# Performance work log

Hardware: AMD Instinct MI355X
Metric: run time of the kernel (lower is better)

Reference implementation:

```python
import jax, jax.numpy as jnp
import numpy as np

NUM_CLASSES = 3
WINDOW = 5.0        # window_size for local connectivity
NUM_ITERS = 5       # mean-field iterations
THETA_BETA = 1.0    # smoothness kernel weight
TEMP = 1.0          # softmax temperature
H, W = 96, 96
B = 1


def setup_inputs() -> dict:
    key = jax.random.key(0)
    unary = jax.random.normal(key, (B, NUM_CLASSES, H, W), dtype=jnp.float32)
    # nn.Parameter(torch.eye(num_classes))
    compatibility = jnp.eye(NUM_CLASSES, dtype=jnp.float32)
    return {"unary": unary, "compatibility": compatibility}


def _pairwise_kernel(h, w):
    """Dense smoothness * local-connectivity kernel [N, N], N = h*w."""
    yy, xx = jnp.meshgrid(jnp.arange(h, dtype=jnp.float32),
                          jnp.arange(w, dtype=jnp.float32), indexing='ij')
    coords = jnp.stack([yy.ravel(), xx.ravel()], axis=-1)          # [N, 2]
    diff = coords[:, None, :] - coords[None, :, :]                 # [N, N, 2]
    dist = jnp.sqrt(jnp.sum(diff * diff, axis=-1))                 # cdist, [N, N]
    n = h * w
    conn = (dist <= WINDOW).astype(jnp.float32)
    conn = conn.at[jnp.arange(n), jnp.arange(n)].set(0.0)          # fill_diagonal_(0)
    smooth = jnp.exp(-THETA_BETA * dist)
    return smooth * conn                                           # [N, N]


def reference(unary, compatibility):
    b, c, h, w = unary.shape
    n = h * w
    unary_flat = unary.reshape(b, c, n)                            # [B, C, N]
    q = jax.nn.softmax(unary_flat / TEMP, axis=1)
    pairwise = _pairwise_kernel(h, w)                              # [N, N] (features=None path)
    for _ in range(NUM_ITERS):
        # messages[b,c,n] = sum_m pairwise[n,m] * q[b,c,m]  (bmm + transpose)
        messages = jnp.einsum('nm,bcm->bcn', pairwise, q)
        comp_msg = jnp.einsum('cd,bdn->bcn', compatibility, messages)
        q = jax.nn.softmax((unary_flat + comp_msg) / TEMP, axis=1)
    return q.reshape(b, c, h, w)
```

## Files before the change

kernel.cpp:

```cpp
#include <hip/hip_runtime.h>


constexpr int HH = 96, WW = 96, NN = HH * WW;
constexpr int TILE = 16, HALO = 5, EXT = TILE + 2 * HALO;

template <bool FIRST, bool LAST>
__global__ __launch_bounds__(TILE * TILE) void crf_iter(
    const float* __restrict__ unary,
    const float* __restrict__ comp,
    const float4* __restrict__ zin,
    float4* __restrict__ zout,
    float* __restrict__ qout)
{
    __shared__ float4 qs[EXT][EXT];
    __shared__ float wtab[121];

    const int tx = threadIdx.x, ty = threadIdx.y;
    const int tid = ty * TILE + tx;

    if (tid < 121) {
        int dy = tid / 11 - 5, dx = tid % 11 - 5;
        int d2 = dy * dy + dx * dx;
        wtab[tid] = (d2 > 0 && d2 <= 25) ? expf(-sqrtf((float)d2)) : 0.0f;
    }

    const int bx0 = blockIdx.x * TILE, by0 = blockIdx.y * TILE;

    for (int i = tid; i < EXT * EXT; i += TILE * TILE) {
        int hy = i / EXT, hx = i - hy * EXT;
        int gy = by0 + hy - HALO, gx = bx0 + hx - HALO;
        float4 q = make_float4(0.f, 0.f, 0.f, 0.f);
        if (gy >= 0 && gy < HH && gx >= 0 && gx < WW) {
            int n = gy * WW + gx;
            float z0, z1, z2;
            if (FIRST) {
                z0 = unary[n];
                z1 = unary[NN + n];
                z2 = unary[2 * NN + n];
            } else {
                float4 z = zin[n];
                z0 = z.x; z1 = z.y; z2 = z.z;
            }
            float mx = fmaxf(z0, fmaxf(z1, z2));
            float e0 = expf(z0 - mx), e1 = expf(z1 - mx), e2 = expf(z2 - mx);
            float inv = 1.0f / (e0 + e1 + e2);
            q = make_float4(e0 * inv, e1 * inv, e2 * inv, 0.f);
        }
        qs[hy][hx] = q;
    }
    __syncthreads();

    float m0 = 0.f, m1 = 0.f, m2 = 0.f;
    constexpr int XLO[11] = {5, 2, 1, 1, 1, 0, 1, 1, 1, 2, 5};
    constexpr int XHI[11] = {5, 8, 9, 9, 9, 10, 9, 9, 9, 8, 5};
#pragma unroll
    for (int dyi = 0; dyi < 11; ++dyi) {
#pragma unroll
        for (int dxi = XLO[dyi]; dxi <= XHI[dyi]; ++dxi) {
            float w = wtab[dyi * 11 + dxi];
            float4 q = qs[ty + dyi][tx + dxi];
            m0 = fmaf(w, q.x, m0);
            m1 = fmaf(w, q.y, m1);
            m2 = fmaf(w, q.z, m2);
        }
    }

    float t0 = comp[0] * m0 + comp[1] * m1 + comp[2] * m2;
    float t1 = comp[3] * m0 + comp[4] * m1 + comp[5] * m2;
    float t2 = comp[6] * m0 + comp[7] * m1 + comp[8] * m2;

    const int n = (by0 + ty) * WW + (bx0 + tx);
    float z0 = unary[n] + t0;
    float z1 = unary[NN + n] + t1;
    float z2 = unary[2 * NN + n] + t2;

    if (LAST) {
        float mx = fmaxf(z0, fmaxf(z1, z2));
        float e0 = expf(z0 - mx), e1 = expf(z1 - mx), e2 = expf(z2 - mx);
        float inv = 1.0f / (e0 + e1 + e2);
        qout[n] = e0 * inv;
        qout[NN + n] = e1 * inv;
        qout[2 * NN + n] = e2 * inv;
    } else {
        zout[n] = make_float4(z0, z1, z2, 0.f);
    }
}

extern "C" void kernel_launch(void* const* d_in, const int* in_sizes, int n_in,
                              void* d_out, int out_size, void* d_ws, size_t ws_size,
                              hipStream_t stream) {
    const float* unary = (const float*)d_in[0];
    const float* comp = (const float*)d_in[1];
    float* out = (float*)d_out;

    float4* zA = (float4*)d_ws;
    float4* zB = zA + NN;

    dim3 grid(WW / TILE, HH / TILE);
    dim3 block(TILE, TILE);

    crf_iter<true,  false><<<grid, block, 0, stream>>>(unary, comp, nullptr, zA, nullptr);
    crf_iter<false, false><<<grid, block, 0, stream>>>(unary, comp, zA, zB, nullptr);
    crf_iter<false, false><<<grid, block, 0, stream>>>(unary, comp, zB, zA, nullptr);
    crf_iter<false, false><<<grid, block, 0, stream>>>(unary, comp, zA, zB, nullptr);
    crf_iter<false, true ><<<grid, block, 0, stream>>>(unary, comp, zB, nullptr, out);
}
```

Before: 81.06 us.

## Fuse five mean-field iterations into one cooperative kernel with grid sync

The five per-iteration launches become a single cooperative kernel. It loops over the iterations and uses a grid-wide barrier between them, since each iteration's halo reads depend on neighbouring blocks' writes. Unary values and the compatibility matrix are loaded into registers once instead of every iteration. This removes repeated launch and teardown overhead, at the cost of cooperative-launch requirements and the latency of a grid barrier across all chiplets.

```diff
diff --git a/kernel.cpp b/kernel.cpp
--- a/kernel.cpp
+++ b/kernel.cpp
@@ -1,17 +1,21 @@
 #include <hip/hip_runtime.h>
+#include <hip/hip_cooperative_groups.h>
+
+namespace cg = cooperative_groups;
 
 
 constexpr int HH = 96, WW = 96, NN = HH * WW;
 constexpr int TILE = 16, HALO = 5, EXT = TILE + 2 * HALO;
 
-template <bool FIRST, bool LAST>
-__global__ __launch_bounds__(TILE * TILE) void crf_iter(
+__global__ __launch_bounds__(TILE * TILE) void crf_fused(
     const float* __restrict__ unary,
     const float* __restrict__ comp,
-    const float4* __restrict__ zin,
-    float4* __restrict__ zout,
+    float4* __restrict__ zA,
+    float4* __restrict__ zB,
     float* __restrict__ qout)
 {
+    cg::grid_group grid = cg::this_grid();
+
     __shared__ float4 qs[EXT][EXT];
     __shared__ float wtab[121];
 
@@ -24,65 +28,78 @@
         wtab[tid] = (d2 > 0 && d2 <= 25) ? expf(-sqrtf((float)d2)) : 0.0f;
     }
 
+    const float c00 = comp[0], c01 = comp[1], c02 = comp[2];
+    const float c10 = comp[3], c11 = comp[4], c12 = comp[5];
+    const float c20 = comp[6], c21 = comp[7], c22 = comp[8];
+
     const int bx0 = blockIdx.x * TILE, by0 = blockIdx.y * TILE;
+    const int n_out = (by0 + ty) * WW + (bx0 + tx);
+    const float u0 = unary[n_out];
+    const float u1 = unary[NN + n_out];
+    const float u2 = unary[2 * NN + n_out];
 
-    for (int i = tid; i < EXT * EXT; i += TILE * TILE) {
-        int hy = i / EXT, hx = i - hy * EXT;
-        int gy = by0 + hy - HALO, gx = bx0 + hx - HALO;
-        float4 q = make_float4(0.f, 0.f, 0.f, 0.f);
-        if (gy >= 0 && gy < HH && gx >= 0 && gx < WW) {
-            int n = gy * WW + gx;
-            float z0, z1, z2;
-            if (FIRST) {
-                z0 = unary[n];
-                z1 = unary[NN + n];
-                z2 = unary[2 * NN + n];
-            } else {
-                float4 z = zin[n];
-                z0 = z.x; z1 = z.y; z2 = z.z;
+    constexpr int XLO[11] = {5, 2, 1, 1, 1, 0, 1, 1, 1, 2, 5};
+    constexpr int XHI[11] = {5, 8, 9, 9, 9, 10, 9, 9, 9, 8, 5};
+
+    for (int it = 0; it < 5; ++it) {
+        const float4* zin = (it & 1) ? zB : zA;
+
+        for (int i = tid; i < EXT * EXT; i += TILE * TILE) {
+            int hy = i / EXT, hx = i - hy * EXT;
+            int gy = by0 + hy - HALO, gx = bx0 + hx - HALO;
+            float4 q = make_float4(0.f, 0.f, 0.f, 0.f);
+            if (gy >= 0 && gy < HH && gx >= 0 && gx < WW) {
+                int n = gy * WW + gx;
+                float z0, z1, z2;
+                if (it == 0) {
+                    z0 = unary[n];
+                    z1 = unary[NN + n];
+                    z2 = unary[2 * NN + n];
+                } else {
+                    float4 z = zin[n];
+                    z0 = z.x; z1 = z.y; z2 = z.z;
+                }
+                float mx = fmaxf(z0, fmaxf(z1, z2));
+                float e0 = expf(z0 - mx), e1 = expf(z1 - mx), e2 = expf(z2 - mx);
+                float inv = 1.0f / (e0 + e1 + e2);
+                q = make_float4(e0 * inv, e1 * inv, e2 * inv, 0.f);
             }
+            qs[hy][hx] = q;
+        }
+        __syncthreads();
+
+        float m0 = 0.f, m1 = 0.f, m2 = 0.f;
+#pragma unroll
+        for (int dyi = 0; dyi < 11; ++dyi) {
+#pragma unroll
+            for (int dxi = XLO[dyi]; dxi <= XHI[dyi]; ++dxi) {
+                float w = wtab[dyi * 11 + dxi];
+                float4 q = qs[ty + dyi][tx + dxi];
+                m0 = fmaf(w, q.x, m0);
+                m1 = fmaf(w, q.y, m1);
+                m2 = fmaf(w, q.z, m2);
+            }
+        }
+
+        float t0 = c00 * m0 + c01 * m1 + c02 * m2;
+        float t1 = c10 * m0 + c11 * m1 + c12 * m2;
+        float t2 = c20 * m0 + c21 * m1 + c22 * m2;
+
+        float z0 = u0 + t0, z1 = u1 + t1, z2 = u2 + t2;
+
+        if (it == 4) {
             float mx = fmaxf(z0, fmaxf(z1, z2));
             float e0 = expf(z0 - mx), e1 = expf(z1 - mx), e2 = expf(z2 - mx);
             float inv = 1.0f / (e0 + e1 + e2);
-            q = make_float4(e0 * inv, e1 * inv, e2 * inv, 0.f);
+            qout[n_out] = e0 * inv;
+            qout[NN + n_out] = e1 * inv;
+            qout[2 * NN + n_out] = e2 * inv;
+        } else {
+            float4* zout = (it & 1) ? zA : zB;
+            zout[n_out] = make_float4(z0, z1, z2, 0.f);
+            __threadfence();
+            grid.sync();
         }
-        qs[hy][hx] = q;
-    }
-    __syncthreads();
-
-    float m0 = 0.f, m1 = 0.f, m2 = 0.f;
-    constexpr int XLO[11] = {5, 2, 1, 1, 1, 0, 1, 1, 1, 2, 5};
-    constexpr int XHI[11] = {5, 8, 9, 9, 9, 10, 9, 9, 9, 8, 5};
-#pragma unroll
-    for (int dyi = 0; dyi < 11; ++dyi) {
-#pragma unroll
-        for (int dxi = XLO[dyi]; dxi <= XHI[dyi]; ++dxi) {
-            float w = wtab[dyi * 11 + dxi];
-            float4 q = qs[ty + dyi][tx + dxi];
-            m0 = fmaf(w, q.x, m0);
-            m1 = fmaf(w, q.y, m1);
-            m2 = fmaf(w, q.z, m2);
-        }
-    }
-
-    float t0 = comp[0] * m0 + comp[1] * m1 + comp[2] * m2;
-    float t1 = comp[3] * m0 + comp[4] * m1 + comp[5] * m2;
-    float t2 = comp[6] * m0 + comp[7] * m1 + comp[8] * m2;
-
-    const int n = (by0 + ty) * WW + (bx0 + tx);
-    float z0 = unary[n] + t0;
-    float z1 = unary[NN + n] + t1;
-    float z2 = unary[2 * NN + n] + t2;
-
-    if (LAST) {
-        float mx = fmaxf(z0, fmaxf(z1, z2));
-        float e0 = expf(z0 - mx), e1 = expf(z1 - mx), e2 = expf(z2 - mx);
-        float inv = 1.0f / (e0 + e1 + e2);
-        qout[n] = e0 * inv;
-        qout[NN + n] = e1 * inv;
-        qout[2 * NN + n] = e2 * inv;
-    } else {
-        zout[n] = make_float4(z0, z1, z2, 0.f);
     }
 }
 
@@ -99,9 +116,6 @@
     dim3 grid(WW / TILE, HH / TILE);
     dim3 block(TILE, TILE);
 
-    crf_iter<true,  false><<<grid, block, 0, stream>>>(unary, comp, nullptr, zA, nullptr);
-    crf_iter<false, false><<<grid, block, 0, stream>>>(unary, comp, zA, zB, nullptr);
-    crf_iter<false, false><<<grid, block, 0, stream>>>(unary, comp, zB, zA, nullptr);
-    crf_iter<false, false><<<grid, block, 0, stream>>>(unary, comp, zA, zB, nullptr);
-    crf_iter<false, true ><<<grid, block, 0, stream>>>(unary, comp, zB, nullptr, out);
+    void* args[] = {(void*)&unary, (void*)&comp, (void*)&zA, (void*)&zB, (void*)&out};
+    hipLaunchCooperativeKernel((const void*)crf_fused, grid, block, args, 0, stream);
 }
```

Measured after the change: 135.4 us. 1.67x slower.

## Fuse multiple mean-field iterations per launch using shrinking-halo temporal blocking

Applied to the files above, without the earlier changes.

Replaces five per-iteration launches with two kernels that run three and two iterations inside shared memory. Each block loads a tile with a halo wide enough for K steps, then recomputes the shrinking region in ping-pong LDS buffers, with a sync between steps. This removes launch overhead and global round-trips between iterations. In exchange it does redundant halo computation, uses more shared memory, and has only 144 small blocks with 8x8 output tiles.

```diff
diff --git a/kernel.cpp b/kernel.cpp
--- a/kernel.cpp
+++ b/kernel.cpp
@@ -2,21 +2,22 @@
 
 
 constexpr int HH = 96, WW = 96, NN = HH * WW;
-constexpr int TILE = 16, HALO = 5, EXT = TILE + 2 * HALO;
+constexpr int T = 8;
 
-template <bool FIRST, bool LAST>
-__global__ __launch_bounds__(TILE * TILE) void crf_iter(
+template <int K, bool FIRST, bool LAST>
+__global__ __launch_bounds__(256) void crf_multi(
     const float* __restrict__ unary,
     const float* __restrict__ comp,
     const float4* __restrict__ zin,
     float4* __restrict__ zout,
     float* __restrict__ qout)
 {
-    __shared__ float4 qs[EXT][EXT];
+    constexpr int EXT = T + 10 * K;
+    __shared__ float4 qa[EXT][EXT + 1];
+    __shared__ float4 qb[EXT][EXT + 1];
     __shared__ float wtab[121];
 
-    const int tx = threadIdx.x, ty = threadIdx.y;
-    const int tid = ty * TILE + tx;
+    const int tid = threadIdx.x;
 
     if (tid < 121) {
         int dy = tid / 11 - 5, dx = tid % 11 - 5;
@@ -24,19 +25,22 @@
         wtab[tid] = (d2 > 0 && d2 <= 25) ? expf(-sqrtf((float)d2)) : 0.0f;
     }
 
-    const int bx0 = blockIdx.x * TILE, by0 = blockIdx.y * TILE;
+    const float c00 = comp[0], c01 = comp[1], c02 = comp[2];
+    const float c10 = comp[3], c11 = comp[4], c12 = comp[5];
+    const float c20 = comp[6], c21 = comp[7], c22 = comp[8];
 
-    for (int i = tid; i < EXT * EXT; i += TILE * TILE) {
+    const int bx0 = blockIdx.x * T - 5 * K;
+    const int by0 = blockIdx.y * T - 5 * K;
+
+    for (int i = tid; i < EXT * EXT; i += 256) {
         int hy = i / EXT, hx = i - hy * EXT;
-        int gy = by0 + hy - HALO, gx = bx0 + hx - HALO;
+        int gy = by0 + hy, gx = bx0 + hx;
         float4 q = make_float4(0.f, 0.f, 0.f, 0.f);
         if (gy >= 0 && gy < HH && gx >= 0 && gx < WW) {
             int n = gy * WW + gx;
             float z0, z1, z2;
             if (FIRST) {
-                z0 = unary[n];
-                z1 = unary[NN + n];
-                z2 = unary[2 * NN + n];
+                z0 = unary[n]; z1 = unary[NN + n]; z2 = unary[2 * NN + n];
             } else {
                 float4 z = zin[n];
                 z0 = z.x; z1 = z.y; z2 = z.z;
@@ -46,43 +50,72 @@
             float inv = 1.0f / (e0 + e1 + e2);
             q = make_float4(e0 * inv, e1 * inv, e2 * inv, 0.f);
         }
-        qs[hy][hx] = q;
+        qa[hy][hx] = q;
     }
     __syncthreads();
 
-    float m0 = 0.f, m1 = 0.f, m2 = 0.f;
     constexpr int XLO[11] = {5, 2, 1, 1, 1, 0, 1, 1, 1, 2, 5};
     constexpr int XHI[11] = {5, 8, 9, 9, 9, 10, 9, 9, 9, 8, 5};
+
 #pragma unroll
-    for (int dyi = 0; dyi < 11; ++dyi) {
+    for (int k = 1; k <= K; ++k) {
+        const int R = T + 10 * (K - k);
+        const int o = 5 * k;
+        const bool rd_a = (k & 1);
+
+        for (int i = tid; i < R * R; i += 256) {
+            int py = i / R, px = i - py * R;
+            int ey = o + py, ex = o + px;
+            int gy = by0 + ey, gx = bx0 + ex;
+            float4 qnew = make_float4(0.f, 0.f, 0.f, 0.f);
+            if (gy >= 0 && gy < HH && gx >= 0 && gx < WW) {
+                float m0 = 0.f, m1 = 0.f, m2 = 0.f;
 #pragma unroll
-        for (int dxi = XLO[dyi]; dxi <= XHI[dyi]; ++dxi) {
-            float w = wtab[dyi * 11 + dxi];
-            float4 q = qs[ty + dyi][tx + dxi];
-            m0 = fmaf(w, q.x, m0);
-            m1 = fmaf(w, q.y, m1);
-            m2 = fmaf(w, q.z, m2);
+                for (int dyi = 0; dyi < 11; ++dyi) {
+#pragma unroll
+                    for (int dxi = XLO[dyi]; dxi <= XHI[dyi]; ++dxi) {
+                        float w = wtab[dyi * 11 + dxi];
+                        float4 q = rd_a ? qa[ey - 5 + dyi][ex - 5 + dxi]
+                                        : qb[ey - 5 + dyi][ex - 5 + dxi];
+                        m0 = fmaf(w, q.x, m0);
+                        m1 = fmaf(w, q.y, m1);
+                        m2 = fmaf(w, q.z, m2);
+                    }
+                }
+                float t0 = c00 * m0 + c01 * m1 + c02 * m2;
+                float t1 = c10 * m0 + c11 * m1 + c12 * m2;
+                float t2 = c20 * m0 + c21 * m1 + c22 * m2;
+
+                int n = gy * WW + gx;
+                float z0 = unary[n] + t0;
+                float z1 = unary[NN + n] + t1;
+                float z2 = unary[2 * NN + n] + t2;
+
+                if (k == K) {
+                    if (LAST) {
+                        float mx = fmaxf(z0, fmaxf(z1, z2));
+                        float e0 = expf(z0 - mx), e1 = expf(z1 - mx),
+                              e2 = expf(z2 - mx);
+                        float inv = 1.0f / (e0 + e1 + e2);
+                        qout[n] = e0 * inv;
+                        qout[NN + n] = e1 * inv;
+                        qout[2 * NN + n] = e2 * inv;
+                    } else {
+                        zout[n] = make_float4(z0, z1, z2, 0.f);
+                    }
+                } else {
+                    float mx = fmaxf(z0, fmaxf(z1, z2));
+                    float e0 = expf(z0 - mx), e1 = expf(z1 - mx),
+                          e2 = expf(z2 - mx);
+                    float inv = 1.0f / (e0 + e1 + e2);
+                    qnew = make_float4(e0 * inv, e1 * inv, e2 * inv, 0.f);
+                }
+            }
+            if (k < K) {
+                if (rd_a) qb[ey][ex] = qnew; else qa[ey][ex] = qnew;
+            }
         }
-    }
-
-    float t0 = comp[0] * m0 + comp[1] * m1 + comp[2] * m2;
-    float t1 = comp[3] * m0 + comp[4] * m1 + comp[5] * m2;
-    float t2 = comp[6] * m0 + comp[7] * m1 + comp[8] * m2;
-
-    const int n = (by0 + ty) * WW + (bx0 + tx);
-    float z0 = unary[n] + t0;
-    float z1 = unary[NN + n] + t1;
-    float z2 = unary[2 * NN + n] + t2;
-
-    if (LAST) {
-        float mx = fmaxf(z0, fmaxf(z1, z2));
-        float e0 = expf(z0 - mx), e1 = expf(z1 - mx), e2 = expf(z2 - mx);
-        float inv = 1.0f / (e0 + e1 + e2);
-        qout[n] = e0 * inv;
-        qout[NN + n] = e1 * inv;
-        qout[2 * NN + n] = e2 * inv;
-    } else {
-        zout[n] = make_float4(z0, z1, z2, 0.f);
+        if (k < K) __syncthreads();
     }
 }
 
@@ -94,14 +127,10 @@
     float* out = (float*)d_out;
 
     float4* zA = (float4*)d_ws;
-    float4* zB = zA + NN;
 
-    dim3 grid(WW / TILE, HH / TILE);
-    dim3 block(TILE, TILE);
+    dim3 grid(WW / T, HH / T);
+    dim3 block(256);
 
-    crf_iter<true,  false><<<grid, block, 0, stream>>>(unary, comp, nullptr, zA, nullptr);
-    crf_iter<false, false><<<grid, block, 0, stream>>>(unary, comp, zA, zB, nullptr);
-    crf_iter<false, false><<<grid, block, 0, stream>>>(unary, comp, zB, zA, nullptr);
-    crf_iter<false, false><<<grid, block, 0, stream>>>(unary, comp, zA, zB, nullptr);
-    crf_iter<false, true ><<<grid, block, 0, stream>>>(unary, comp, zB, nullptr, out);
+    crf_multi<3, true,  false><<<grid, block, 0, stream>>>(unary, comp, nullptr, zA, nullptr);
+    crf_multi<2, false, true ><<<grid, block, 0, stream>>>(unary, comp, zA, nullptr, out);
 }
```

Result: slower. 92.46 us (+14.1%).

## Shrink tiles to 8x8 for more blocks and store softmaxed q between iterations

Applied to the files above, without the earlier changes.

Tiles drop from 16x16 to 8x8 with 64-thread blocks, which raises the grid from 36 to 144 blocks and fills more of the GPU's compute units. The intermediate buffer now holds the already-softmaxed q instead of raw logits, so the halo load no longer recomputes exp and the division for every halo pixel. Shared memory gets one column of padding, and the compatibility matrix is loaded into registers up front. The cost is a larger halo fraction (18x18 loads for 64 outputs) and more redundant global reads.

```diff
diff --git a/kernel.cpp b/kernel.cpp
--- a/kernel.cpp
+++ b/kernel.cpp
@@ -2,54 +2,55 @@
 
 
 constexpr int HH = 96, WW = 96, NN = HH * WW;
-constexpr int TILE = 16, HALO = 5, EXT = TILE + 2 * HALO;
+constexpr int T = 8, HALO = 5, EXT = T + 2 * HALO;
 
 template <bool FIRST, bool LAST>
-__global__ __launch_bounds__(TILE * TILE) void crf_iter(
+__global__ __launch_bounds__(64) void crf_iter(
     const float* __restrict__ unary,
     const float* __restrict__ comp,
-    const float4* __restrict__ zin,
-    float4* __restrict__ zout,
+    const float4* __restrict__ qin,
+    float4* __restrict__ qnext,
     float* __restrict__ qout)
 {
-    __shared__ float4 qs[EXT][EXT];
+    __shared__ float4 qs[EXT][EXT + 1];
     __shared__ float wtab[121];
 
-    const int tx = threadIdx.x, ty = threadIdx.y;
-    const int tid = ty * TILE + tx;
+    const int tid = threadIdx.x;
 
-    if (tid < 121) {
-        int dy = tid / 11 - 5, dx = tid % 11 - 5;
+    for (int i = tid; i < 121; i += 64) {
+        int dy = i / 11 - 5, dx = i % 11 - 5;
         int d2 = dy * dy + dx * dx;
-        wtab[tid] = (d2 > 0 && d2 <= 25) ? expf(-sqrtf((float)d2)) : 0.0f;
+        wtab[i] = (d2 > 0 && d2 <= 25) ? expf(-sqrtf((float)d2)) : 0.0f;
     }
 
-    const int bx0 = blockIdx.x * TILE, by0 = blockIdx.y * TILE;
+    const float c00 = comp[0], c01 = comp[1], c02 = comp[2];
+    const float c10 = comp[3], c11 = comp[4], c12 = comp[5];
+    const float c20 = comp[6], c21 = comp[7], c22 = comp[8];
 
-    for (int i = tid; i < EXT * EXT; i += TILE * TILE) {
+    const int bx0 = blockIdx.x * T - HALO;
+    const int by0 = blockIdx.y * T - HALO;
+
+    for (int i = tid; i < EXT * EXT; i += 64) {
         int hy = i / EXT, hx = i - hy * EXT;
-        int gy = by0 + hy - HALO, gx = bx0 + hx - HALO;
+        int gy = by0 + hy, gx = bx0 + hx;
         float4 q = make_float4(0.f, 0.f, 0.f, 0.f);
         if (gy >= 0 && gy < HH && gx >= 0 && gx < WW) {
             int n = gy * WW + gx;
-            float z0, z1, z2;
             if (FIRST) {
-                z0 = unary[n];
-                z1 = unary[NN + n];
-                z2 = unary[2 * NN + n];
+                float z0 = unary[n], z1 = unary[NN + n], z2 = unary[2 * NN + n];
+                float mx = fmaxf(z0, fmaxf(z1, z2));
+                float e0 = expf(z0 - mx), e1 = expf(z1 - mx), e2 = expf(z2 - mx);
+                float inv = 1.0f / (e0 + e1 + e2);
+                q = make_float4(e0 * inv, e1 * inv, e2 * inv, 0.f);
             } else {
-                float4 z = zin[n];
-                z0 = z.x; z1 = z.y; z2 = z.z;
+                q = qin[n];
             }
-            float mx = fmaxf(z0, fmaxf(z1, z2));
-            float e0 = expf(z0 - mx), e1 = expf(z1 - mx), e2 = expf(z2 - mx);
-            float inv = 1.0f / (e0 + e1 + e2);
-            q = make_float4(e0 * inv, e1 * inv, e2 * inv, 0.f);
         }
         qs[hy][hx] = q;
     }
     __syncthreads();
 
+    const int ty = tid >> 3, tx = tid & 7;
     float m0 = 0.f, m1 = 0.f, m2 = 0.f;
     constexpr int XLO[11] = {5, 2, 1, 1, 1, 0, 1, 1, 1, 2, 5};
     constexpr int XHI[11] = {5, 8, 9, 9, 9, 10, 9, 9, 9, 8, 5};
@@ -65,24 +66,25 @@
         }
     }
 
-    float t0 = comp[0] * m0 + comp[1] * m1 + comp[2] * m2;
-    float t1 = comp[3] * m0 + comp[4] * m1 + comp[5] * m2;
-    float t2 = comp[6] * m0 + comp[7] * m1 + comp[8] * m2;
+    float t0 = c00 * m0 + c01 * m1 + c02 * m2;
+    float t1 = c10 * m0 + c11 * m1 + c12 * m2;
+    float t2 = c20 * m0 + c21 * m1 + c22 * m2;
 
-    const int n = (by0 + ty) * WW + (bx0 + tx);
+    const int n = (blockIdx.y * T + ty) * WW + (blockIdx.x * T + tx);
     float z0 = unary[n] + t0;
     float z1 = unary[NN + n] + t1;
     float z2 = unary[2 * NN + n] + t2;
 
+    float mx = fmaxf(z0, fmaxf(z1, z2));
+    float e0 = expf(z0 - mx), e1 = expf(z1 - mx), e2 = expf(z2 - mx);
+    float inv = 1.0f / (e0 + e1 + e2);
+
     if (LAST) {
-        float mx = fmaxf(z0, fmaxf(z1, z2));
-        float e0 = expf(z0 - mx), e1 = expf(z1 - mx), e2 = expf(z2 - mx);
-        float inv = 1.0f / (e0 + e1 + e2);
         qout[n] = e0 * inv;
         qout[NN + n] = e1 * inv;
         qout[2 * NN + n] = e2 * inv;
     } else {
-        zout[n] = make_float4(z0, z1, z2, 0.f);
+        qnext[n] = make_float4(e0 * inv, e1 * inv, e2 * inv, 0.f);
     }
 }
 
@@ -93,15 +95,15 @@
     const float* comp = (const float*)d_in[1];
     float* out = (float*)d_out;
 
-    float4* zA = (float4*)d_ws;
-    float4* zB = zA + NN;
+    float4* qA = (float4*)d_ws;
+    float4* qB = qA + NN;
 
-    dim3 grid(WW / TILE, HH / TILE);
-    dim3 block(TILE, TILE);
+    dim3 grid(WW / T, HH / T);
+    dim3 block(64);
 
-    crf_iter<true,  false><<<grid, block, 0, stream>>>(unary, comp, nullptr, zA, nullptr);
-    crf_iter<false, false><<<grid, block, 0, stream>>>(unary, comp, zA, zB, nullptr);
-    crf_iter<false, false><<<grid, block, 0, stream>>>(unary, comp, zB, zA, nullptr);
-    crf_iter<false, false><<<grid, block, 0, stream>>>(unary, comp, zA, zB, nullptr);
-    crf_iter<false, true ><<<grid, block, 0, stream>>>(unary, comp, zB, nullptr, out);
+    crf_iter<true,  false><<<grid, block, 0, stream>>>(unary, comp, nullptr, qA, nullptr);
+    crf_iter<false, false><<<grid, block, 0, stream>>>(unary, comp, qA, qB, nullptr);
+    crf_iter<false, false><<<grid, block, 0, stream>>>(unary, comp, qB, qA, nullptr);
+    crf_iter<false, false><<<grid, block, 0, stream>>>(unary, comp, qA, qB, nullptr);
+    crf_iter<false, true ><<<grid, block, 0, stream>>>(unary, comp, qB, nullptr, out);
 }
```

Result: no change. 79.70 us, median of 2 (-1.7%).
